# Performance work log

Measured on AMD Instinct MI355X. Metric: run time of the kernel, lower is better.

Reference implementation:

```python
import jax, jax.numpy as jnp
import numpy as np

B, H, W, C = 64, 32, 32, 256
HZ, WZ = 16, 16
N = 64          # hidden_dim = n_proposals
K = 3           # dynamic depthwise kernel size
EPS = 1e-5


def _layernorm(x, g, b):
    mu = jnp.mean(x, axis=-1, keepdims=True)
    var = jnp.var(x, axis=-1, keepdims=True)
    return (x - mu) * jax.lax.rsqrt(var + EPS) * g + b


def setup_inputs() -> dict:
    key = jax.random.key(0)
    ks = jax.random.split(key, 8)
    s = 0.02  # weight init scale
    return {
        "x_feat": jax.random.normal(ks[0], (B, H, W, C), jnp.float32),
        "z_feat": jax.random.normal(ks[1], (B, HZ, WZ, C), jnp.float32),
        "Wz": jax.random.normal(ks[2], (C, N), jnp.float32) * s,
        "bz": jnp.zeros((N,), jnp.float32),
        "Wx": jax.random.normal(ks[3], (C, N), jnp.float32) * s,
        "bx": jnp.zeros((N,), jnp.float32),
        "Wdyn": jax.random.normal(ks[4], (C, N + K), jnp.float32) * s,
        "bdyn": jnp.zeros((N + K,), jnp.float32),
        "g_norm": jnp.ones((C,), jnp.float32),
        "b_norm": jnp.zeros((C,), jnp.float32),
        "Wp": jax.random.normal(ks[5], (C, 1), jnp.float32) * s,
        "bp": jnp.zeros((1,), jnp.float32),
        "g_ln": jnp.ones((C,), jnp.float32),
        "b_ln": jnp.zeros((C,), jnp.float32),
    }


def _dysep_conv_atten(query, value, Wdyn, bdyn, g_norm, b_norm):
    # query, value: [B, N, C]
    dy = query @ Wdyn + bdyn                      # [B, N, N+K]
    w_depth = dy[:, :, :K]                        # [B, N, K] per-channel depthwise kernels
    w_point = dy[:, :, K:]                        # [B, N, N] per-sample pointwise (1x1) weights
    # depthwise conv along C with 'same' padding (torch conv1d = cross-correlation)
    vpad = jnp.pad(value, ((0, 0), (0, 0), (1, 1)))
    depth = (w_depth[..., 0:1] * vpad[:, :, 0:C]
             + w_depth[..., 1:2] * vpad[:, :, 1:C + 1]
             + w_depth[..., 2:3] * vpad[:, :, 2:C + 2])
    depth = jax.nn.relu(depth)                    # [B, N, C]
    point = jnp.einsum('bnm,bmc->bnc', w_point, depth)
    return _layernorm(point, g_norm, b_norm)


def reference(x_feat, z_feat, Wz, bz, Wx, bx, Wdyn, bdyn,
              g_norm, b_norm, Wp, bp, g_ln, b_ln):
    # kernels from template features (detached in the original: kernels.detach())
    z_core = z_feat @ Wz + bz                                   # [B,HZ,WZ,N]
    kernels = jnp.einsum('bhwn,bhwc->bnc', z_core, z_feat)      # [B,N,C]
    kernels = jax.lax.stop_gradient(kernels)

    x_n = x_feat @ Wx + bx                                      # [B,H,W,N]
    kernels_x = jnp.einsum('bhwn,bhwc->bnc', x_n, x_feat)       # [B,N,C]
    kernels_x = _dysep_conv_atten(kernels, kernels_x, Wdyn, bdyn, g_norm, b_norm)

    x_corr = jnp.einsum('bnc,bhwn->bhwc', kernels_x, x_n)       # [B,H,W,C]
    proto = kernels_x @ Wp + bp                                 # [B,N,1]
    tem = jax.nn.sigmoid(jnp.einsum('bnd,bnc->bdc', proto, kernels_x))  # [B,1,C]
    tem = tem[:, :, None, :]                                    # [B,1,1,C]
    x_corr = x_corr * tem

    return x_feat + jax.nn.relu(_layernorm(x_corr, g_ln, b_ln))
```

## Files before the change

### kernel.cpp

```cpp
#include <hip/hip_runtime.h>
#include <math.h>

#define EPSV 1e-5f

__global__ __launch_bounds__(256) void gemm_all(
    const float* __restrict__ Xx, const float* __restrict__ Wxp,
    const float* __restrict__ bxp, float* __restrict__ Yx,
    const float* __restrict__ Xz, const float* __restrict__ Wzp,
    const float* __restrict__ bzp, float* __restrict__ Yz)
{
    __shared__ float Xc[16][64];
    __shared__ float Wc[16][64];
    const int t = threadIdx.x;
    const float *X, *W, *bias; float* Y; long r0;
    if (blockIdx.x < 1024) { X = Xx; W = Wxp; bias = bxp; Y = Yx; r0 = (long)blockIdx.x * 64; }
    else                   { X = Xz; W = Wzp; bias = bzp; Y = Yz; r0 = (long)(blockIdx.x - 1024) * 64; }

    const int tr = t >> 4, tc = t & 15;
    float4 bv = *(const float4*)(bias + tc * 4);
    float acc[4][4];
#pragma unroll
    for (int i = 0; i < 4; ++i) { acc[i][0]=bv.x; acc[i][1]=bv.y; acc[i][2]=bv.z; acc[i][3]=bv.w; }

    const int lr = t >> 2, lc = (t & 3) * 4;
    const int wl = t >> 4, wj = (t & 15) * 4;
    float4 xv = *(const float4*)(X + (r0 + lr) * 256 + lc);
    float4 wv = *(const float4*)(W + (long)wl * 64 + wj);

    for (int c0 = 0; c0 < 256; c0 += 16) {
        Xc[lc + 0][lr] = xv.x; Xc[lc + 1][lr] = xv.y; Xc[lc + 2][lr] = xv.z; Xc[lc + 3][lr] = xv.w;
        *(float4*)&Wc[wl][wj] = wv;
        __syncthreads();
        if (c0 + 16 < 256) {
            xv = *(const float4*)(X + (r0 + lr) * 256 + c0 + 16 + lc);
            wv = *(const float4*)(W + (long)(c0 + 16 + wl) * 64 + wj);
        }
#pragma unroll
        for (int cl = 0; cl < 16; ++cl) {
            float4 a = *(float4*)&Xc[cl][tr * 4];
            float4 b = *(float4*)&Wc[cl][tc * 4];
            acc[0][0] += a.x * b.x; acc[0][1] += a.x * b.y; acc[0][2] += a.x * b.z; acc[0][3] += a.x * b.w;
            acc[1][0] += a.y * b.x; acc[1][1] += a.y * b.y; acc[1][2] += a.y * b.z; acc[1][3] += a.y * b.w;
            acc[2][0] += a.z * b.x; acc[2][1] += a.z * b.y; acc[2][2] += a.z * b.z; acc[2][3] += a.z * b.w;
            acc[3][0] += a.w * b.x; acc[3][1] += a.w * b.y; acc[3][2] += a.w * b.z; acc[3][3] += a.w * b.w;
        }
        __syncthreads();
    }
#pragma unroll
    for (int i = 0; i < 4; ++i) {
        float4 o = make_float4(acc[i][0], acc[i][1], acc[i][2], acc[i][3]);
        *(float4*)(Y + (r0 + tr * 4 + i) * 64 + tc * 4) = o;
    }
}

__global__ __launch_bounds__(256) void corr_all(
    const float* __restrict__ xn, const float* __restrict__ xf,
    float* __restrict__ kxr, const float* __restrict__ zc,
    const float* __restrict__ zf, float* __restrict__ kern)
{
    __shared__ float A[16 * 64];
    __shared__ float Bt[16 * 64];
    const int t = threadIdx.x;
    const float *Yn, *X; float* S; int b, P;
    if (blockIdx.y < 64) { b = blockIdx.y;      Yn = xn; X = xf; S = kxr;  P = 1024; }
    else                 { b = blockIdx.y - 64; Yn = zc; X = zf; S = kern; P = 256;  }
    const int c0 = blockIdx.x * 64;
    const int lp = t >> 4, lj = (t & 15) * 4;
    const int tn = t >> 4, tc = t & 15;

    float acc[4][4] = {};
    long rb = (long)b * P + lp;
    float4 av = *(const float4*)(Yn + rb * 64 + lj);
    float4 bv = *(const float4*)(X + rb * 256 + c0 + lj);

    for (int p0 = 0; p0 < P; p0 += 16) {
        *(float4*)&A[lp * 64 + lj] = av;
        *(float4*)&Bt[lp * 64 + lj] = bv;
        __syncthreads();
        if (p0 + 16 < P) {
            long rb2 = (long)b * P + p0 + 16 + lp;
            av = *(const float4*)(Yn + rb2 * 64 + lj);
            bv = *(const float4*)(X + rb2 * 256 + c0 + lj);
        }
#pragma unroll
        for (int p = 0; p < 16; ++p) {
            float4 a = *(float4*)&A[p * 64 + tn * 4];
            float4 b4 = *(float4*)&Bt[p * 64 + tc * 4];
            acc[0][0] += a.x * b4.x; acc[0][1] += a.x * b4.y; acc[0][2] += a.x * b4.z; acc[0][3] += a.x * b4.w;
            acc[1][0] += a.y * b4.x; acc[1][1] += a.y * b4.y; acc[1][2] += a.y * b4.z; acc[1][3] += a.y * b4.w;
            acc[2][0] += a.z * b4.x; acc[2][1] += a.z * b4.y; acc[2][2] += a.z * b4.z; acc[2][3] += a.z * b4.w;
            acc[3][0] += a.w * b4.x; acc[3][1] += a.w * b4.y; acc[3][2] += a.w * b4.z; acc[3][3] += a.w * b4.w;
        }
        __syncthreads();
    }
#pragma unroll
    for (int i = 0; i < 4; ++i) {
        float4 o = make_float4(acc[i][0], acc[i][1], acc[i][2], acc[i][3]);
        *(float4*)(S + ((long)(b * 64 + tn * 4 + i)) * 256 + c0 + tc * 4) = o;
    }
}

__global__ __launch_bounds__(256) void pointln_tem(
    const float* __restrict__ kern, const float* __restrict__ Wdyn,
    const float* __restrict__ bdyn, const float* __restrict__ v,
    const float* __restrict__ g, const float* __restrict__ bta,
    const float* __restrict__ Wp, const float* __restrict__ bp,
    float* __restrict__ pointbuf, float* __restrict__ kx,
    float* __restrict__ tem)
{
    __shared__ float wp[64][64];
    __shared__ float Ac[16][64];
    __shared__ float Wc[16][64];
    __shared__ float wd[64][4];
    __shared__ float red1[64][4], red2[64][4];
    __shared__ float mu[64], rr[64], proto[64];
    const int b = blockIdx.x, t = threadIdx.x;
    const int tr = t >> 4, tc = t & 15;

    {
        float acc[4][4];
#pragma unroll
        for (int j = 0; j < 4; ++j) {
            float bj = bdyn[3 + tc * 4 + j];
            acc[0][j] = bj; acc[1][j] = bj; acc[2][j] = bj; acc[3][j] = bj;
        }
        const int lr = t >> 2, lc = (t & 3) * 4;
        const int wl = t >> 4, wj = (t & 15) * 4;
        float4 av = *(const float4*)(kern + ((long)(b * 64 + lr)) * 256 + lc);
        float w0 = Wdyn[wl * 67 + 3 + wj + 0];
        float w1 = Wdyn[wl * 67 + 3 + wj + 1];
        float w2 = Wdyn[wl * 67 + 3 + wj + 2];
        float w3 = Wdyn[wl * 67 + 3 + wj + 3];
        for (int c0 = 0; c0 < 256; c0 += 16) {
            Ac[lc + 0][lr] = av.x; Ac[lc + 1][lr] = av.y; Ac[lc + 2][lr] = av.z; Ac[lc + 3][lr] = av.w;
            Wc[wl][wj + 0] = w0; Wc[wl][wj + 1] = w1; Wc[wl][wj + 2] = w2; Wc[wl][wj + 3] = w3;
            __syncthreads();
            if (c0 + 16 < 256) {
                av = *(const float4*)(kern + ((long)(b * 64 + lr)) * 256 + c0 + 16 + lc);
                w0 = Wdyn[(c0 + 16 + wl) * 67 + 3 + wj + 0];
                w1 = Wdyn[(c0 + 16 + wl) * 67 + 3 + wj + 1];
                w2 = Wdyn[(c0 + 16 + wl) * 67 + 3 + wj + 2];
                w3 = Wdyn[(c0 + 16 + wl) * 67 + 3 + wj + 3];
            }
#pragma unroll
            for (int cl = 0; cl < 16; ++cl) {
                float4 a = *(float4*)&Ac[cl][tr * 4];
                float4 w = *(float4*)&Wc[cl][tc * 4];
                acc[0][0] += a.x * w.x; acc[0][1] += a.x * w.y; acc[0][2] += a.x * w.z; acc[0][3] += a.x * w.w;
                acc[1][0] += a.y * w.x; acc[1][1] += a.y * w.y; acc[1][2] += a.y * w.z; acc[1][3] += a.y * w.w;
                acc[2][0] += a.z * w.x; acc[2][1] += a.z * w.y; acc[2][2] += a.z * w.z; acc[2][3] += a.z * w.w;
                acc[3][0] += a.w * w.x; acc[3][1] += a.w * w.y; acc[3][2] += a.w * w.z; acc[3][3] += a.w * w.w;
            }
            __syncthreads();
        }
#pragma unroll
        for (int i = 0; i < 4; ++i)
            *(float4*)&wp[tr * 4 + i][tc * 4] = make_float4(acc[i][0], acc[i][1], acc[i][2], acc[i][3]);
    }
    if (t < 192) {
        int n = t / 3, j = t - n * 3;
        const float* kr = kern + ((long)(b * 64 + n)) * 256;
        float a0 = 0.f, a1 = 0.f, a2 = 0.f, a3 = 0.f;
        for (int c = 0; c < 256; c += 4) {
            a0 += kr[c + 0] * Wdyn[(c + 0) * 67 + j];
            a1 += kr[c + 1] * Wdyn[(c + 1) * 67 + j];
            a2 += kr[c + 2] * Wdyn[(c + 2) * 67 + j];
            a3 += kr[c + 3] * Wdyn[(c + 3) * 67 + j];
        }
        wd[n][j] = a0 + a1 + a2 + a3 + bdyn[j];
    }
    __syncthreads();

    const int c = t;
    float dcol[64];
#pragma unroll
    for (int m = 0; m < 64; ++m) {
        const float* vr = v + ((long)(b * 64 + m)) * 256;
        float vm = (c > 0)   ? vr[c - 1] : 0.f;
        float v0 = vr[c];
        float vp = (c < 255) ? vr[c + 1] : 0.f;
        float d = wd[m][0] * vm + wd[m][1] * v0 + wd[m][2] * vp;
        dcol[m] = fmaxf(d, 0.f);
    }
#pragma unroll 4
    for (int n = 0; n < 64; ++n) {
        float a = 0.f;
#pragma unroll
        for (int m4 = 0; m4 < 16; ++m4) {
            float4 w = *(float4*)&wp[n][m4 * 4];
            a += w.x * dcol[m4 * 4 + 0] + w.y * dcol[m4 * 4 + 1]
               + w.z * dcol[m4 * 4 + 2] + w.w * dcol[m4 * 4 + 3];
        }
        pointbuf[((long)(b * 64 + n)) * 256 + c] = a;
    }
    __syncthreads();
    {
        int n = t >> 2, q = t & 3;
        const float* pr = pointbuf + ((long)(b * 64 + n)) * 256 + q * 64;
        float s = 0.f, s2 = 0.f;
        for (int k = 0; k < 64; ++k) { float x = pr[k]; s += x; s2 += x * x; }
        red1[n][q] = s; red2[n][q] = s2;
    }
    __syncthreads();
    if (t < 64) {
        float s  = red1[t][0] + red1[t][1] + red1[t][2] + red1[t][3];
        float s2 = red2[t][0] + red2[t][1] + red2[t][2] + red2[t][3];
        float m = s * (1.f / 256.f);
        mu[t] = m; rr[t] = rsqrtf(s2 * (1.f / 256.f) - m * m + EPSV);
    }
    __syncthreads();
    {
        float gc = g[c], bc = bta[c];
#pragma unroll 4
        for (int n = 0; n < 64; ++n) {
            long off = ((long)(b * 64 + n)) * 256 + c;
            kx[off] = (pointbuf[off] - mu[n]) * rr[n] * gc + bc;
        }
    }
    __syncthreads();
    {
        int n = t >> 2, q = t & 3;
        const float* kr = kx + ((long)(b * 64 + n)) * 256 + q * 64;
        const float* wr = Wp + q * 64;
        float s = 0.f;
        for (int k = 0; k < 64; ++k) s += kr[k] * wr[k];
        red1[n][q] = s;
    }
    __syncthreads();
    if (t < 64) proto[t] = red1[t][0] + red1[t][1] + red1[t][2] + red1[t][3] + bp[0];
    __syncthreads();
    {
        float s = 0.f;
#pragma unroll 4
        for (int n = 0; n < 64; ++n) s += proto[n] * kx[((long)(b * 64 + n)) * 256 + c];
        tem[b * 256 + c] = 1.f / (1.f + expf(-s));
    }
}

__global__ __launch_bounds__(256) void final_kernel(
    const float* __restrict__ xn, const float* __restrict__ kx,
    const float* __restrict__ tem, const float* __restrict__ xf,
    const float* __restrict__ g, const float* __restrict__ bt,
    float* __restrict__ out)
{
    __shared__ float xtT[64][68];
    __shared__ float kc[64][68];
    __shared__ float rs1[64][17], rs2[64][17];
    __shared__ float mu[64], rr[64];
    const int t = threadIdx.x;
    const int b = blockIdx.y;
    const int pg = blockIdx.x;
    const int tr = t >> 4;
    const int tc = t & 15;

    {
        int row = t >> 2, q = t & 3;
        const float* src = xn + ((long)(b * 1024 + pg * 64 + row)) * 64 + q * 16;
        float4 f0 = *(const float4*)(src + 0);
        float4 f1 = *(const float4*)(src + 4);
        float4 f2 = *(const float4*)(src + 8);
        float4 f3 = *(const float4*)(src + 12);
        int n0 = q * 16;
        xtT[n0 + 0][row] = f0.x; xtT[n0 + 1][row] = f0.y; xtT[n0 + 2][row] = f0.z; xtT[n0 + 3][row] = f0.w;
        xtT[n0 + 4][row] = f1.x; xtT[n0 + 5][row] = f1.y; xtT[n0 + 6][row] = f1.z; xtT[n0 + 7][row] = f1.w;
        xtT[n0 + 8][row] = f2.x; xtT[n0 + 9][row] = f2.y; xtT[n0 +10][row] = f2.z; xtT[n0 +11][row] = f2.w;
        xtT[n0 +12][row] = f3.x; xtT[n0 +13][row] = f3.y; xtT[n0 +14][row] = f3.z; xtT[n0 +15][row] = f3.w;
    }

    float4 xcv[4][4];
    float si[4] = {0.f, 0.f, 0.f, 0.f}, s2i[4] = {0.f, 0.f, 0.f, 0.f};
#pragma unroll
    for (int cc = 0; cc < 4; ++cc) {
        __syncthreads();
#pragma unroll
        for (int i = 0; i < 4; ++i) {
            int idx = t + i * 256;
            int n = idx >> 4, jq = idx & 15;
            *(float4*)&kc[n][jq * 4] =
                *(const float4*)(kx + ((long)(b * 64 + n)) * 256 + cc * 64 + jq * 4);
        }
        __syncthreads();
        float4 a0 = {0,0,0,0}, a1 = {0,0,0,0}, a2 = {0,0,0,0}, a3 = {0,0,0,0};
#pragma unroll 8
        for (int n = 0; n < 64; ++n) {
            float4 xv = *(float4*)&xtT[n][tr * 4];
            float4 kv = *(float4*)&kc[n][tc * 4];
            a0.x += xv.x * kv.x; a0.y += xv.x * kv.y; a0.z += xv.x * kv.z; a0.w += xv.x * kv.w;
            a1.x += xv.y * kv.x; a1.y += xv.y * kv.y; a1.z += xv.y * kv.z; a1.w += xv.y * kv.w;
            a2.x += xv.z * kv.x; a2.y += xv.z * kv.y; a2.z += xv.z * kv.z; a2.w += xv.z * kv.w;
            a3.x += xv.w * kv.x; a3.y += xv.w * kv.y; a3.z += xv.w * kv.z; a3.w += xv.w * kv.w;
        }
        float4 tv = *(const float4*)(tem + b * 256 + cc * 64 + tc * 4);
        a0.x *= tv.x; a0.y *= tv.y; a0.z *= tv.z; a0.w *= tv.w;
        a1.x *= tv.x; a1.y *= tv.y; a1.z *= tv.z; a1.w *= tv.w;
        a2.x *= tv.x; a2.y *= tv.y; a2.z *= tv.z; a2.w *= tv.w;
        a3.x *= tv.x; a3.y *= tv.y; a3.z *= tv.z; a3.w *= tv.w;
        xcv[cc][0] = a0; xcv[cc][1] = a1; xcv[cc][2] = a2; xcv[cc][3] = a3;
        si[0]  += a0.x + a0.y + a0.z + a0.w;  s2i[0] += a0.x*a0.x + a0.y*a0.y + a0.z*a0.z + a0.w*a0.w;
        si[1]  += a1.x + a1.y + a1.z + a1.w;  s2i[1] += a1.x*a1.x + a1.y*a1.y + a1.z*a1.z + a1.w*a1.w;
        si[2]  += a2.x + a2.y + a2.z + a2.w;  s2i[2] += a2.x*a2.x + a2.y*a2.y + a2.z*a2.z + a2.w*a2.w;
        si[3]  += a3.x + a3.y + a3.z + a3.w;  s2i[3] += a3.x*a3.x + a3.y*a3.y + a3.z*a3.z + a3.w*a3.w;
    }
#pragma unroll
    for (int i = 0; i < 4; ++i) { rs1[tr * 4 + i][tc] = si[i]; rs2[tr * 4 + i][tc] = s2i[i]; }
    __syncthreads();
    if (t < 64) {
        float s = 0.f, s2 = 0.f;
#pragma unroll
        for (int k = 0; k < 16; ++k) { s += rs1[t][k]; s2 += rs2[t][k]; }
        float m = s * (1.f / 256.f);
        mu[t] = m; rr[t] = rsqrtf(s2 * (1.f / 256.f) - m * m + EPSV);
    }
    __syncthreads();
#pragma unroll
    for (int cc = 0; cc < 4; ++cc) {
        int cb = cc * 64 + tc * 4;
        float4 g4 = *(const float4*)(g + cb);
        float4 b4 = *(const float4*)(bt + cb);
#pragma unroll
        for (int i = 0; i < 4; ++i) {
            int row = tr * 4 + i;
            float m = mu[row], r = rr[row];
            long grow = ((long)(b * 1024 + pg * 64 + row)) * 256;
            float4 xfv = *(const float4*)(xf + grow + cb);
            float4 a = xcv[cc][i];
            float4 o;
            o.x = xfv.x + fmaxf((a.x - m) * r * g4.x + b4.x, 0.f);
            o.y = xfv.y + fmaxf((a.y - m) * r * g4.y + b4.y, 0.f);
            o.z = xfv.z + fmaxf((a.z - m) * r * g4.z + b4.z, 0.f);
            o.w = xfv.w + fmaxf((a.w - m) * r * g4.w + b4.w, 0.f);
            *(float4*)(out + grow + cb) = o;
        }
    }
}

extern "C" void kernel_launch(void* const* d_in, const int* in_sizes, int n_in,
                              void* d_out, int out_size, void* d_ws, size_t ws_size,
                              hipStream_t stream)
{
    (void)in_sizes; (void)n_in; (void)out_size; (void)ws_size;
    const float* x_feat = (const float*)d_in[0];
    const float* z_feat = (const float*)d_in[1];
    const float* Wz     = (const float*)d_in[2];
    const float* bz     = (const float*)d_in[3];
    const float* Wx     = (const float*)d_in[4];
    const float* bx     = (const float*)d_in[5];
    const float* Wdyn   = (const float*)d_in[6];
    const float* bdyn   = (const float*)d_in[7];
    const float* g_norm = (const float*)d_in[8];
    const float* b_norm = (const float*)d_in[9];
    const float* Wp     = (const float*)d_in[10];
    const float* bp     = (const float*)d_in[11];
    const float* g_ln   = (const float*)d_in[12];
    const float* b_ln   = (const float*)d_in[13];
    float* out = (float*)d_out;

    float* ws   = (float*)d_ws;
    float* xn   = ws;
    float* zc   = xn + 4194304;
    float* kern = zc + 1048576;
    float* kxr  = kern + 1048576;
    float* kx   = kxr + 1048576;
    float* temb = kx + 1048576;

    gemm_all<<<1280, 256, 0, stream>>>(x_feat, Wx, bx, xn, z_feat, Wz, bz, zc);
    corr_all<<<dim3(4, 128), 256, 0, stream>>>(xn, x_feat, kxr, zc, z_feat, kern);
    pointln_tem<<<64, 256, 0, stream>>>(kern, Wdyn, bdyn, kxr, g_norm, b_norm,
                                        Wp, bp, zc, kx, temb);
    final_kernel<<<dim3(16, 64), 256, 0, stream>>>(xn, kx, temb, x_feat, g_ln, b_ln, out);
}
```

Baseline: 314.7 us.

## Split dynamic-conv stage into parallel kernels, fold layernorm and tem into final

The single 64-block pointln_tem kernel is replaced by three kernels: dy_all computes the dynamic weights, depthpoint runs the depthwise conv and pointwise GEMM over a 4x64 grid and emits partial row statistics, and lntem finishes the layernorm statistics and the sigmoid gate analytically as per-channel scale and shift. final_kernel now applies the layernorm and gate while it stages the kernels, so the normalized kx buffer is no longer materialized. gemm_all moves to 128-row tiles with 8x4 per-thread outputs, and corr_all stages 64-row K tiles instead of 16. The aim is more parallelism in the low-occupancy middle stage and fewer barriers and better reuse in the GEMMs, at the cost of two extra launches and larger shared-memory use.

New measurement: 324.6 us. 3.1% more time.

```diff
diff --git a/kernel.cpp b/kernel.cpp
--- a/kernel.cpp
+++ b/kernel.cpp
@@ -9,47 +9,58 @@
     const float* __restrict__ Xz, const float* __restrict__ Wzp,
     const float* __restrict__ bzp, float* __restrict__ Yz)
 {
-    __shared__ float Xc[16][64];
-    __shared__ float Wc[16][64];
+    __shared__ float Xc[16 * 132];
+    __shared__ float Wc[16 * 64];
     const int t = threadIdx.x;
     const float *X, *W, *bias; float* Y; long r0;
-    if (blockIdx.x < 1024) { X = Xx; W = Wxp; bias = bxp; Y = Yx; r0 = (long)blockIdx.x * 64; }
-    else                   { X = Xz; W = Wzp; bias = bzp; Y = Yz; r0 = (long)(blockIdx.x - 1024) * 64; }
+    if (blockIdx.x < 512) { X = Xx; W = Wxp; bias = bxp; Y = Yx; r0 = (long)blockIdx.x * 128; }
+    else                  { X = Xz; W = Wzp; bias = bzp; Y = Yz; r0 = (long)(blockIdx.x - 512) * 128; }
 
     const int tr = t >> 4, tc = t & 15;
     float4 bv = *(const float4*)(bias + tc * 4);
-    float acc[4][4];
-#pragma unroll
-    for (int i = 0; i < 4; ++i) { acc[i][0]=bv.x; acc[i][1]=bv.y; acc[i][2]=bv.z; acc[i][3]=bv.w; }
-
-    const int lr = t >> 2, lc = (t & 3) * 4;
+    float acc[8][4];
+#pragma unroll
+    for (int i = 0; i < 8; ++i) { acc[i][0]=bv.x; acc[i][1]=bv.y; acc[i][2]=bv.z; acc[i][3]=bv.w; }
+
+    const int lr = t >> 2;
+    const int lc = (t & 3) * 4;
     const int wl = t >> 4, wj = (t & 15) * 4;
-    float4 xv = *(const float4*)(X + (r0 + lr) * 256 + lc);
-    float4 wv = *(const float4*)(W + (long)wl * 64 + wj);
+    float4 xv0 = *(const float4*)(X + (r0 + lr) * 256 + lc);
+    float4 xv1 = *(const float4*)(X + (r0 + lr + 64) * 256 + lc);
+    float4 wv  = *(const float4*)(W + (long)wl * 64 + wj);
 
     for (int c0 = 0; c0 < 256; c0 += 16) {
-        Xc[lc + 0][lr] = xv.x; Xc[lc + 1][lr] = xv.y; Xc[lc + 2][lr] = xv.z; Xc[lc + 3][lr] = xv.w;
-        *(float4*)&Wc[wl][wj] = wv;
+        Xc[(lc+0)*132 + lr] = xv0.x; Xc[(lc+1)*132 + lr] = xv0.y;
+        Xc[(lc+2)*132 + lr] = xv0.z; Xc[(lc+3)*132 + lr] = xv0.w;
+        Xc[(lc+0)*132 + lr+64] = xv1.x; Xc[(lc+1)*132 + lr+64] = xv1.y;
+        Xc[(lc+2)*132 + lr+64] = xv1.z; Xc[(lc+3)*132 + lr+64] = xv1.w;
+        *(float4*)&Wc[wl * 64 + wj] = wv;
         __syncthreads();
         if (c0 + 16 < 256) {
-            xv = *(const float4*)(X + (r0 + lr) * 256 + c0 + 16 + lc);
-            wv = *(const float4*)(W + (long)(c0 + 16 + wl) * 64 + wj);
+            xv0 = *(const float4*)(X + (r0 + lr) * 256 + c0 + 16 + lc);
+            xv1 = *(const float4*)(X + (r0 + lr + 64) * 256 + c0 + 16 + lc);
+            wv  = *(const float4*)(W + (long)(c0 + 16 + wl) * 64 + wj);
         }
 #pragma unroll
         for (int cl = 0; cl < 16; ++cl) {
-            float4 a = *(float4*)&Xc[cl][tr * 4];
-            float4 b = *(float4*)&Wc[cl][tc * 4];
-            acc[0][0] += a.x * b.x; acc[0][1] += a.x * b.y; acc[0][2] += a.x * b.z; acc[0][3] += a.x * b.w;
-            acc[1][0] += a.y * b.x; acc[1][1] += a.y * b.y; acc[1][2] += a.y * b.z; acc[1][3] += a.y * b.w;
-            acc[2][0] += a.z * b.x; acc[2][1] += a.z * b.y; acc[2][2] += a.z * b.z; acc[2][3] += a.z * b.w;
-            acc[3][0] += a.w * b.x; acc[3][1] += a.w * b.y; acc[3][2] += a.w * b.z; acc[3][3] += a.w * b.w;
-        }
-        __syncthreads();
-    }
-#pragma unroll
-    for (int i = 0; i < 4; ++i) {
+            float4 a0 = *(float4*)&Xc[cl * 132 + tr * 8];
+            float4 a1 = *(float4*)&Xc[cl * 132 + tr * 8 + 4];
+            float4 b4 = *(float4*)&Wc[cl * 64 + tc * 4];
+            acc[0][0]+=a0.x*b4.x; acc[0][1]+=a0.x*b4.y; acc[0][2]+=a0.x*b4.z; acc[0][3]+=a0.x*b4.w;
+            acc[1][0]+=a0.y*b4.x; acc[1][1]+=a0.y*b4.y; acc[1][2]+=a0.y*b4.z; acc[1][3]+=a0.y*b4.w;
+            acc[2][0]+=a0.z*b4.x; acc[2][1]+=a0.z*b4.y; acc[2][2]+=a0.z*b4.z; acc[2][3]+=a0.z*b4.w;
+            acc[3][0]+=a0.w*b4.x; acc[3][1]+=a0.w*b4.y; acc[3][2]+=a0.w*b4.z; acc[3][3]+=a0.w*b4.w;
+            acc[4][0]+=a1.x*b4.x; acc[4][1]+=a1.x*b4.y; acc[4][2]+=a1.x*b4.z; acc[4][3]+=a1.x*b4.w;
+            acc[5][0]+=a1.y*b4.x; acc[5][1]+=a1.y*b4.y; acc[5][2]+=a1.y*b4.z; acc[5][3]+=a1.y*b4.w;
+            acc[6][0]+=a1.z*b4.x; acc[6][1]+=a1.z*b4.y; acc[6][2]+=a1.z*b4.z; acc[6][3]+=a1.z*b4.w;
+            acc[7][0]+=a1.w*b4.x; acc[7][1]+=a1.w*b4.y; acc[7][2]+=a1.w*b4.z; acc[7][3]+=a1.w*b4.w;
+        }
+        __syncthreads();
+    }
+#pragma unroll
+    for (int i = 0; i < 8; ++i) {
         float4 o = make_float4(acc[i][0], acc[i][1], acc[i][2], acc[i][3]);
-        *(float4*)(Y + (r0 + tr * 4 + i) * 64 + tc * 4) = o;
+        *(float4*)(Y + (r0 + tr * 8 + i) * 64 + tc * 4) = o;
     }
 }
 
@@ -58,38 +69,49 @@
     float* __restrict__ kxr, const float* __restrict__ zc,
     const float* __restrict__ zf, float* __restrict__ kern)
 {
-    __shared__ float A[16 * 64];
-    __shared__ float Bt[16 * 64];
+    __shared__ float A[64 * 64];
+    __shared__ float Bt[64 * 64];
     const int t = threadIdx.x;
     const float *Yn, *X; float* S; int b, P;
     if (blockIdx.y < 64) { b = blockIdx.y;      Yn = xn; X = xf; S = kxr;  P = 1024; }
     else                 { b = blockIdx.y - 64; Yn = zc; X = zf; S = kern; P = 256;  }
     const int c0 = blockIdx.x * 64;
-    const int lp = t >> 4, lj = (t & 15) * 4;
     const int tn = t >> 4, tc = t & 15;
 
     float acc[4][4] = {};
-    long rb = (long)b * P + lp;
-    float4 av = *(const float4*)(Yn + rb * 64 + lj);
-    float4 bv = *(const float4*)(X + rb * 256 + c0 + lj);
-
-    for (int p0 = 0; p0 < P; p0 += 16) {
-        *(float4*)&A[lp * 64 + lj] = av;
-        *(float4*)&Bt[lp * 64 + lj] = bv;
-        __syncthreads();
-        if (p0 + 16 < P) {
-            long rb2 = (long)b * P + p0 + 16 + lp;
-            av = *(const float4*)(Yn + rb2 * 64 + lj);
-            bv = *(const float4*)(X + rb2 * 256 + c0 + lj);
-        }
-#pragma unroll
-        for (int p = 0; p < 16; ++p) {
-            float4 a = *(float4*)&A[p * 64 + tn * 4];
+    float4 av[4], bv4[4];
+#pragma unroll
+    for (int i = 0; i < 4; ++i) {
+        int idx = t + i * 256; int p = idx >> 4, f4 = (idx & 15) * 4;
+        long rb = (long)b * P + p;
+        av[i]  = *(const float4*)(Yn + rb * 64 + f4);
+        bv4[i] = *(const float4*)(X + rb * 256 + c0 + f4);
+    }
+    for (int p0 = 0; p0 < P; p0 += 64) {
+#pragma unroll
+        for (int i = 0; i < 4; ++i) {
+            int idx = t + i * 256; int p = idx >> 4, f4 = (idx & 15) * 4;
+            *(float4*)&A[p * 64 + f4] = av[i];
+            *(float4*)&Bt[p * 64 + f4] = bv4[i];
+        }
+        __syncthreads();
+        if (p0 + 64 < P) {
+#pragma unroll
+            for (int i = 0; i < 4; ++i) {
+                int idx = t + i * 256; int p = idx >> 4, f4 = (idx & 15) * 4;
+                long rb = (long)b * P + p0 + 64 + p;
+                av[i]  = *(const float4*)(Yn + rb * 64 + f4);
+                bv4[i] = *(const float4*)(X + rb * 256 + c0 + f4);
+            }
+        }
+#pragma unroll 16
+        for (int p = 0; p < 64; ++p) {
+            float4 a  = *(float4*)&A[p * 64 + tn * 4];
             float4 b4 = *(float4*)&Bt[p * 64 + tc * 4];
-            acc[0][0] += a.x * b4.x; acc[0][1] += a.x * b4.y; acc[0][2] += a.x * b4.z; acc[0][3] += a.x * b4.w;
-            acc[1][0] += a.y * b4.x; acc[1][1] += a.y * b4.y; acc[1][2] += a.y * b4.z; acc[1][3] += a.y * b4.w;
-            acc[2][0] += a.z * b4.x; acc[2][1] += a.z * b4.y; acc[2][2] += a.z * b4.z; acc[2][3] += a.z * b4.w;
-            acc[3][0] += a.w * b4.x; acc[3][1] += a.w * b4.y; acc[3][2] += a.w * b4.z; acc[3][3] += a.w * b4.w;
+            acc[0][0]+=a.x*b4.x; acc[0][1]+=a.x*b4.y; acc[0][2]+=a.x*b4.z; acc[0][3]+=a.x*b4.w;
+            acc[1][0]+=a.y*b4.x; acc[1][1]+=a.y*b4.y; acc[1][2]+=a.y*b4.z; acc[1][3]+=a.y*b4.w;
+            acc[2][0]+=a.z*b4.x; acc[2][1]+=a.z*b4.y; acc[2][2]+=a.z*b4.z; acc[2][3]+=a.z*b4.w;
+            acc[3][0]+=a.w*b4.x; acc[3][1]+=a.w*b4.y; acc[3][2]+=a.w*b4.z; acc[3][3]+=a.w*b4.w;
         }
         __syncthreads();
     }
@@ -100,159 +122,247 @@
     }
 }
 
-__global__ __launch_bounds__(256) void pointln_tem(
+__global__ __launch_bounds__(256) void dy_all(
     const float* __restrict__ kern, const float* __restrict__ Wdyn,
-    const float* __restrict__ bdyn, const float* __restrict__ v,
+    const float* __restrict__ bdyn, float* __restrict__ dyb)
+{
+    __shared__ float Ac[16 * 64];
+    __shared__ float Wc[16 * 64];
+    __shared__ float Wd3[48];
+    const int b = blockIdx.x, t = threadIdx.x;
+    const int tr = t >> 4, tc = t & 15;
+    float acc[4][4];
+#pragma unroll
+    for (int j = 0; j < 4; ++j) {
+        float bj = bdyn[3 + tc * 4 + j];
+        acc[0][j] = bj; acc[1][j] = bj; acc[2][j] = bj; acc[3][j] = bj;
+    }
+    const int lr = t >> 2, lc = (t & 3) * 4;
+    const int wl = t >> 4, wj = (t & 15) * 4;
+    const int nwd = t / 3, jwd = t - nwd * 3;
+    float wdacc = 0.f;
+    float4 av = *(const float4*)(kern + ((long)(b * 64 + lr)) * 256 + lc);
+    float w0 = Wdyn[wl * 67 + 3 + wj + 0];
+    float w1 = Wdyn[wl * 67 + 3 + wj + 1];
+    float w2 = Wdyn[wl * 67 + 3 + wj + 2];
+    float w3 = Wdyn[wl * 67 + 3 + wj + 3];
+    float wdr = (t < 48) ? Wdyn[(t / 3) * 67 + (t % 3)] : 0.f;
+
+    for (int c0 = 0; c0 < 256; c0 += 16) {
+        Ac[(lc+0)*64 + lr] = av.x; Ac[(lc+1)*64 + lr] = av.y;
+        Ac[(lc+2)*64 + lr] = av.z; Ac[(lc+3)*64 + lr] = av.w;
+        Wc[wl*64 + wj+0] = w0; Wc[wl*64 + wj+1] = w1;
+        Wc[wl*64 + wj+2] = w2; Wc[wl*64 + wj+3] = w3;
+        if (t < 48) Wd3[t] = wdr;
+        __syncthreads();
+        if (c0 + 16 < 256) {
+            av = *(const float4*)(kern + ((long)(b * 64 + lr)) * 256 + c0 + 16 + lc);
+            w0 = Wdyn[(c0 + 16 + wl) * 67 + 3 + wj + 0];
+            w1 = Wdyn[(c0 + 16 + wl) * 67 + 3 + wj + 1];
+            w2 = Wdyn[(c0 + 16 + wl) * 67 + 3 + wj + 2];
+            w3 = Wdyn[(c0 + 16 + wl) * 67 + 3 + wj + 3];
+            if (t < 48) wdr = Wdyn[(c0 + 16 + t / 3) * 67 + (t % 3)];
+        }
+#pragma unroll
+        for (int cl = 0; cl < 16; ++cl) {
+            float4 a = *(float4*)&Ac[cl * 64 + tr * 4];
+            float4 w = *(float4*)&Wc[cl * 64 + tc * 4];
+            acc[0][0]+=a.x*w.x; acc[0][1]+=a.x*w.y; acc[0][2]+=a.x*w.z; acc[0][3]+=a.x*w.w;
+            acc[1][0]+=a.y*w.x; acc[1][1]+=a.y*w.y; acc[1][2]+=a.y*w.z; acc[1][3]+=a.y*w.w;
+            acc[2][0]+=a.z*w.x; acc[2][1]+=a.z*w.y; acc[2][2]+=a.z*w.z; acc[2][3]+=a.z*w.w;
+            acc[3][0]+=a.w*w.x; acc[3][1]+=a.w*w.y; acc[3][2]+=a.w*w.z; acc[3][3]+=a.w*w.w;
+        }
+        if (t < 192) {
+#pragma unroll
+            for (int cl = 0; cl < 16; ++cl)
+                wdacc += Ac[cl * 64 + nwd] * Wd3[cl * 3 + jwd];
+        }
+        __syncthreads();
+    }
+#pragma unroll
+    for (int i = 0; i < 4; ++i) {
+        float4 o = make_float4(acc[i][0], acc[i][1], acc[i][2], acc[i][3]);
+        *(float4*)(dyb + ((long)(b * 64 + tr * 4 + i)) * 68 + tc * 4) = o;
+    }
+    if (t < 192) dyb[((long)(b * 64 + nwd)) * 68 + 64 + jwd] = wdacc + bdyn[jwd];
+}
+
+__global__ __launch_bounds__(256) void depthpoint(
+    const float* __restrict__ dyb, const float* __restrict__ v,
+    const float* __restrict__ g, const float* __restrict__ Wp,
+    float* __restrict__ point, float* __restrict__ partials)
+{
+    __shared__ float smem[13312];
+    float* wpT = smem;
+    float* wd3 = smem + 4352;
+    float* vt  = smem + 4608;
+    float* dep = smem + 8960;
+    float* rs  = vt;
+
+    const int t = threadIdx.x;
+    const int b = blockIdx.y, ct = blockIdx.x, c0 = ct * 64;
+    const int tr = t >> 4, tc = t & 15;
+
+#pragma unroll
+    for (int i = 0; i < 4; ++i) {
+        int idx = t + i * 256; int n = idx >> 4, m0 = (idx & 15) * 4;
+        float4 w4 = *(const float4*)(dyb + ((long)(b * 64 + n)) * 68 + m0);
+        wpT[(m0+0)*68 + n] = w4.x; wpT[(m0+1)*68 + n] = w4.y;
+        wpT[(m0+2)*68 + n] = w4.z; wpT[(m0+3)*68 + n] = w4.w;
+    }
+    if (t < 64) {
+        long o = ((long)(b * 64 + t)) * 68 + 64;
+        wd3[t*4+0] = dyb[o+0]; wd3[t*4+1] = dyb[o+1]; wd3[t*4+2] = dyb[o+2];
+    }
+    {
+        int m = t >> 2, lc0 = (t & 3) * 17;
+#pragma unroll
+        for (int k = 0; k < 17; ++k) {
+            int lc = lc0 + k;
+            if (lc < 66) {
+                int c = c0 - 1 + lc;
+                vt[m * 68 + lc] = (c >= 0 && c < 256) ? v[((long)(b * 64 + m)) * 256 + c] : 0.f;
+            }
+        }
+    }
+    __syncthreads();
+#pragma unroll
+    for (int im = 0; im < 4; ++im) {
+        int m = tr * 4 + im;
+        float w0 = wd3[m*4+0], w1 = wd3[m*4+1], w2 = wd3[m*4+2];
+#pragma unroll
+        for (int jc = 0; jc < 4; ++jc) {
+            int cl = tc * 4 + jc;
+            float d = w0 * vt[m*68 + cl] + w1 * vt[m*68 + cl + 1] + w2 * vt[m*68 + cl + 2];
+            dep[m*68 + cl] = fmaxf(d, 0.f);
+        }
+    }
+    __syncthreads();
+    float acc[4][4] = {};
+#pragma unroll 16
+    for (int m = 0; m < 64; ++m) {
+        float4 a4 = *(float4*)&wpT[m * 68 + tr * 4];
+        float4 d4 = *(float4*)&dep[m * 68 + tc * 4];
+        acc[0][0]+=a4.x*d4.x; acc[0][1]+=a4.x*d4.y; acc[0][2]+=a4.x*d4.z; acc[0][3]+=a4.x*d4.w;
+        acc[1][0]+=a4.y*d4.x; acc[1][1]+=a4.y*d4.y; acc[1][2]+=a4.y*d4.z; acc[1][3]+=a4.y*d4.w;
+        acc[2][0]+=a4.z*d4.x; acc[2][1]+=a4.z*d4.y; acc[2][2]+=a4.z*d4.z; acc[2][3]+=a4.z*d4.w;
+        acc[3][0]+=a4.w*d4.x; acc[3][1]+=a4.w*d4.y; acc[3][2]+=a4.w*d4.z; acc[3][3]+=a4.w*d4.w;
+    }
+    int cg = c0 + tc * 4;
+    float4 g4  = *(const float4*)(g + cg);
+    float4 wp4 = *(const float4*)(Wp + cg);
+    float gw0 = g4.x*wp4.x, gw1 = g4.y*wp4.y, gw2 = g4.z*wp4.z, gw3 = g4.w*wp4.w;
+#pragma unroll
+    for (int i = 0; i < 4; ++i) {
+        float4 o = make_float4(acc[i][0], acc[i][1], acc[i][2], acc[i][3]);
+        *(float4*)(point + ((long)(b * 64 + tr * 4 + i)) * 256 + cg) = o;
+        float s  = o.x + o.y + o.z + o.w;
+        float s2 = o.x*o.x + o.y*o.y + o.z*o.z + o.w*o.w;
+        float dg = o.x*gw0 + o.y*gw1 + o.z*gw2 + o.w*gw3;
+        rs[0*1088 + (tr*4+i)*17 + tc] = s;
+        rs[1*1088 + (tr*4+i)*17 + tc] = s2;
+        rs[2*1088 + (tr*4+i)*17 + tc] = dg;
+    }
+    __syncthreads();
+    if (t < 64) {
+        float s = 0.f, s2 = 0.f, dg = 0.f;
+#pragma unroll
+        for (int j = 0; j < 16; ++j) {
+            s  += rs[t*17 + j];
+            s2 += rs[1088 + t*17 + j];
+            dg += rs[2176 + t*17 + j];
+        }
+        long base = ((long)(b * 4 + ct)) * 192;
+        partials[base + t]        = s;
+        partials[base + 64 + t]   = s2;
+        partials[base + 128 + t]  = dg;
+    }
+}
+
+__global__ __launch_bounds__(256) void lntem(
+    const float* __restrict__ partials, const float* __restrict__ point,
     const float* __restrict__ g, const float* __restrict__ bta,
     const float* __restrict__ Wp, const float* __restrict__ bp,
-    float* __restrict__ pointbuf, float* __restrict__ kx,
-    float* __restrict__ tem)
-{
-    __shared__ float wp[64][64];
-    __shared__ float Ac[16][64];
-    __shared__ float Wc[16][64];
-    __shared__ float wd[64][4];
-    __shared__ float red1[64][4], red2[64][4];
-    __shared__ float mu[64], rr[64], proto[64];
+    float* __restrict__ murr, float* __restrict__ AB)
+{
+    __shared__ float sA[256], sB[256];
+    __shared__ float wnv[64];
+    __shared__ float tot[4];
     const int b = blockIdx.x, t = threadIdx.x;
-    const int tr = t >> 4, tc = t & 15;
-
-    {
-        float acc[4][4];
-#pragma unroll
-        for (int j = 0; j < 4; ++j) {
-            float bj = bdyn[3 + tc * 4 + j];
-            acc[0][j] = bj; acc[1][j] = bj; acc[2][j] = bj; acc[3][j] = bj;
-        }
-        const int lr = t >> 2, lc = (t & 3) * 4;
-        const int wl = t >> 4, wj = (t & 15) * 4;
-        float4 av = *(const float4*)(kern + ((long)(b * 64 + lr)) * 256 + lc);
-        float w0 = Wdyn[wl * 67 + 3 + wj + 0];
-        float w1 = Wdyn[wl * 67 + 3 + wj + 1];
-        float w2 = Wdyn[wl * 67 + 3 + wj + 2];
-        float w3 = Wdyn[wl * 67 + 3 + wj + 3];
-        for (int c0 = 0; c0 < 256; c0 += 16) {
-            Ac[lc + 0][lr] = av.x; Ac[lc + 1][lr] = av.y; Ac[lc + 2][lr] = av.z; Ac[lc + 3][lr] = av.w;
-            Wc[wl][wj + 0] = w0; Wc[wl][wj + 1] = w1; Wc[wl][wj + 2] = w2; Wc[wl][wj + 3] = w3;
-            __syncthreads();
-            if (c0 + 16 < 256) {
-                av = *(const float4*)(kern + ((long)(b * 64 + lr)) * 256 + c0 + 16 + lc);
-                w0 = Wdyn[(c0 + 16 + wl) * 67 + 3 + wj + 0];
-                w1 = Wdyn[(c0 + 16 + wl) * 67 + 3 + wj + 1];
-                w2 = Wdyn[(c0 + 16 + wl) * 67 + 3 + wj + 2];
-                w3 = Wdyn[(c0 + 16 + wl) * 67 + 3 + wj + 3];
-            }
-#pragma unroll
-            for (int cl = 0; cl < 16; ++cl) {
-                float4 a = *(float4*)&Ac[cl][tr * 4];
-                float4 w = *(float4*)&Wc[cl][tc * 4];
-                acc[0][0] += a.x * w.x; acc[0][1] += a.x * w.y; acc[0][2] += a.x * w.z; acc[0][3] += a.x * w.w;
-                acc[1][0] += a.y * w.x; acc[1][1] += a.y * w.y; acc[1][2] += a.y * w.z; acc[1][3] += a.y * w.w;
-                acc[2][0] += a.z * w.x; acc[2][1] += a.z * w.y; acc[2][2] += a.z * w.z; acc[2][3] += a.z * w.w;
-                acc[3][0] += a.w * w.x; acc[3][1] += a.w * w.y; acc[3][2] += a.w * w.z; acc[3][3] += a.w * w.w;
-            }
-            __syncthreads();
-        }
-#pragma unroll
-        for (int i = 0; i < 4; ++i)
-            *(float4*)&wp[tr * 4 + i][tc * 4] = make_float4(acc[i][0], acc[i][1], acc[i][2], acc[i][3]);
-    }
-    if (t < 192) {
-        int n = t / 3, j = t - n * 3;
-        const float* kr = kern + ((long)(b * 64 + n)) * 256;
-        float a0 = 0.f, a1 = 0.f, a2 = 0.f, a3 = 0.f;
-        for (int c = 0; c < 256; c += 4) {
-            a0 += kr[c + 0] * Wdyn[(c + 0) * 67 + j];
-            a1 += kr[c + 1] * Wdyn[(c + 1) * 67 + j];
-            a2 += kr[c + 2] * Wdyn[(c + 2) * 67 + j];
-            a3 += kr[c + 3] * Wdyn[(c + 3) * 67 + j];
-        }
-        wd[n][j] = a0 + a1 + a2 + a3 + bdyn[j];
-    }
-    __syncthreads();
-
     const int c = t;
-    float dcol[64];
-#pragma unroll
-    for (int m = 0; m < 64; ++m) {
-        const float* vr = v + ((long)(b * 64 + m)) * 256;
-        float vm = (c > 0)   ? vr[c - 1] : 0.f;
-        float v0 = vr[c];
-        float vp = (c < 255) ? vr[c + 1] : 0.f;
-        float d = wd[m][0] * vm + wd[m][1] * v0 + wd[m][2] * vp;
-        dcol[m] = fmaxf(d, 0.f);
-    }
-#pragma unroll 4
-    for (int n = 0; n < 64; ++n) {
-        float a = 0.f;
-#pragma unroll
-        for (int m4 = 0; m4 < 16; ++m4) {
-            float4 w = *(float4*)&wp[n][m4 * 4];
-            a += w.x * dcol[m4 * 4 + 0] + w.y * dcol[m4 * 4 + 1]
-               + w.z * dcol[m4 * 4 + 2] + w.w * dcol[m4 * 4 + 3];
-        }
-        pointbuf[((long)(b * 64 + n)) * 256 + c] = a;
-    }
-    __syncthreads();
-    {
-        int n = t >> 2, q = t & 3;
-        const float* pr = pointbuf + ((long)(b * 64 + n)) * 256 + q * 64;
-        float s = 0.f, s2 = 0.f;
-        for (int k = 0; k < 64; ++k) { float x = pr[k]; s += x; s2 += x * x; }
-        red1[n][q] = s; red2[n][q] = s2;
-    }
-    __syncthreads();
+    float gc = g[c], bc = bta[c], wpc = Wp[c];
+    sA[t] = gc * wpc; sB[t] = bc * wpc;
+    __syncthreads();
+    for (int off = 128; off >= 1; off >>= 1) {
+        if (t < off) { sA[t] += sA[t+off]; sB[t] += sB[t+off]; }
+        __syncthreads();
+    }
+    if (t == 0) { tot[0] = sA[0]; tot[1] = sB[0] + bp[0]; }
+    __syncthreads();
+    float Sgw = tot[0], Sbw = tot[1];
+
+    float protoe = 0.f, mu = 0.f, rr = 0.f;
     if (t < 64) {
-        float s  = red1[t][0] + red1[t][1] + red1[t][2] + red1[t][3];
-        float s2 = red2[t][0] + red2[t][1] + red2[t][2] + red2[t][3];
-        float m = s * (1.f / 256.f);
-        mu[t] = m; rr[t] = rsqrtf(s2 * (1.f / 256.f) - m * m + EPSV);
-    }
-    __syncthreads();
-    {
-        float gc = g[c], bc = bta[c];
-#pragma unroll 4
-        for (int n = 0; n < 64; ++n) {
-            long off = ((long)(b * 64 + n)) * 256 + c;
-            kx[off] = (pointbuf[off] - mu[n]) * rr[n] * gc + bc;
-        }
-    }
-    __syncthreads();
-    {
-        int n = t >> 2, q = t & 3;
-        const float* kr = kx + ((long)(b * 64 + n)) * 256 + q * 64;
-        const float* wr = Wp + q * 64;
-        float s = 0.f;
-        for (int k = 0; k < 64; ++k) s += kr[k] * wr[k];
-        red1[n][q] = s;
-    }
-    __syncthreads();
-    if (t < 64) proto[t] = red1[t][0] + red1[t][1] + red1[t][2] + red1[t][3] + bp[0];
-    __syncthreads();
-    {
-        float s = 0.f;
-#pragma unroll 4
-        for (int n = 0; n < 64; ++n) s += proto[n] * kx[((long)(b * 64 + n)) * 256 + c];
-        tem[b * 256 + c] = 1.f / (1.f + expf(-s));
-    }
+        float S1 = 0.f, S2 = 0.f, Sdg = 0.f;
+#pragma unroll
+        for (int ct = 0; ct < 4; ++ct) {
+            long o = ((long)(b * 4 + ct)) * 192;
+            S1 += partials[o + t]; S2 += partials[o + 64 + t]; Sdg += partials[o + 128 + t];
+        }
+        mu = S1 * (1.f / 256.f);
+        float var = S2 * (1.f / 256.f) - mu * mu;
+        rr = rsqrtf(var + EPSV);
+        protoe = rr * (Sdg - mu * Sgw) + Sbw;
+        wnv[t] = protoe * rr;
+        murr[b * 128 + 2*t]     = rr;
+        murr[b * 128 + 2*t + 1] = -mu * rr;
+    }
+    __syncthreads();
+    sA[t] = (t < 64) ? protoe * rr * mu : 0.f;
+    sB[t] = (t < 64) ? protoe : 0.f;
+    __syncthreads();
+    for (int off = 128; off >= 1; off >>= 1) {
+        if (t < off) { sA[t] += sA[t+off]; sB[t] += sB[t+off]; }
+        __syncthreads();
+    }
+    if (t == 0) { tot[2] = sA[0]; tot[3] = sB[0]; }
+    __syncthreads();
+    float Bv = tot[2], Sv = tot[3];
+
+    const float* pcol = point + (long)b * 64 * 256 + c;
+    float a0 = 0.f, a1 = 0.f, a2 = 0.f, a3 = 0.f;
+#pragma unroll
+    for (int n = 0; n < 64; n += 4) {
+        a0 += wnv[n+0] * pcol[(n+0) * 256];
+        a1 += wnv[n+1] * pcol[(n+1) * 256];
+        a2 += wnv[n+2] * pcol[(n+2) * 256];
+        a3 += wnv[n+3] * pcol[(n+3) * 256];
+    }
+    float accA = a0 + a1 + a2 + a3;
+    float x = gc * (accA - Bv) + bc * Sv;
+    float temv = 1.f / (1.f + expf(-x));
+    AB[b * 512 + c]       = gc * temv;
+    AB[b * 512 + 256 + c] = bc * temv;
 }
 
 __global__ __launch_bounds__(256) void final_kernel(
-    const float* __restrict__ xn, const float* __restrict__ kx,
-    const float* __restrict__ tem, const float* __restrict__ xf,
-    const float* __restrict__ g, const float* __restrict__ bt,
-    float* __restrict__ out)
-{
-    __shared__ float xtT[64][68];
-    __shared__ float kc[64][68];
-    __shared__ float rs1[64][17], rs2[64][17];
+    const float* __restrict__ xn, const float* __restrict__ point,
+    const float* __restrict__ murr, const float* __restrict__ AB,
+    const float* __restrict__ xf, const float* __restrict__ g,
+    const float* __restrict__ bt, float* __restrict__ out)
+{
+    __shared__ float xtT[64 * 68];
+    __shared__ float kc[64 * 68];
+    __shared__ float rs1[64 * 17], rs2[64 * 17];
     __shared__ float mu[64], rr[64];
+    __shared__ float rq[128];
     const int t = threadIdx.x;
     const int b = blockIdx.y;
     const int pg = blockIdx.x;
     const int tr = t >> 4;
     const int tc = t & 15;
 
+    if (t < 128) rq[t] = murr[b * 128 + t];
     {
         int row = t >> 2, q = t & 3;
         const float* src = xn + ((long)(b * 1024 + pg * 64 + row)) * 64 + q * 16;
@@ -261,14 +371,14 @@
         float4 f2 = *(const float4*)(src + 8);
         float4 f3 = *(const float4*)(src + 12);
         int n0 = q * 16;
-        xtT[n0 + 0][row] = f0.x; xtT[n0 + 1][row] = f0.y; xtT[n0 + 2][row] = f0.z; xtT[n0 + 3][row] = f0.w;
-        xtT[n0 + 4][row] = f1.x; xtT[n0 + 5][row] = f1.y; xtT[n0 + 6][row] = f1.z; xtT[n0 + 7][row] = f1.w;
-        xtT[n0 + 8][row] = f2.x; xtT[n0 + 9][row] = f2.y; xtT[n0 +10][row] = f2.z; xtT[n0 +11][row] = f2.w;
-        xtT[n0 +12][row] = f3.x; xtT[n0 +13][row] = f3.y; xtT[n0 +14][row] = f3.z; xtT[n0 +15][row] = f3.w;
+        xtT[(n0+ 0)*68+row]=f0.x; xtT[(n0+ 1)*68+row]=f0.y; xtT[(n0+ 2)*68+row]=f0.z; xtT[(n0+ 3)*68+row]=f0.w;
+        xtT[(n0+ 4)*68+row]=f1.x; xtT[(n0+ 5)*68+row]=f1.y; xtT[(n0+ 6)*68+row]=f1.z; xtT[(n0+ 7)*68+row]=f1.w;
+        xtT[(n0+ 8)*68+row]=f2.x; xtT[(n0+ 9)*68+row]=f2.y; xtT[(n0+10)*68+row]=f2.z; xtT[(n0+11)*68+row]=f2.w;
+        xtT[(n0+12)*68+row]=f3.x; xtT[(n0+13)*68+row]=f3.y; xtT[(n0+14)*68+row]=f3.z; xtT[(n0+15)*68+row]=f3.w;
     }
 
     float4 xcv[4][4];
-    float si[4] = {0.f, 0.f, 0.f, 0.f}, s2i[4] = {0.f, 0.f, 0.f, 0.f};
+    float si[4] = {0.f,0.f,0.f,0.f}, s2i[4] = {0.f,0.f,0.f,0.f};
 #pragma unroll
     for (int cc = 0; cc < 4; ++cc) {
         __syncthreads();
@@ -276,38 +386,42 @@
         for (int i = 0; i < 4; ++i) {
             int idx = t + i * 256;
             int n = idx >> 4, jq = idx & 15;
-            *(float4*)&kc[n][jq * 4] =
-                *(const float4*)(kx + ((long)(b * 64 + n)) * 256 + cc * 64 + jq * 4);
+            int cb = cc * 64 + jq * 4;
+            float4 p4 = *(const float4*)(point + ((long)(b * 64 + n)) * 256 + cb);
+            float rn = rq[2*n], qn = rq[2*n + 1];
+            float4 A4 = *(const float4*)(AB + b * 512 + cb);
+            float4 B4 = *(const float4*)(AB + b * 512 + 256 + cb);
+            float4 kv;
+            kv.x = (p4.x * rn + qn) * A4.x + B4.x;
+            kv.y = (p4.y * rn + qn) * A4.y + B4.y;
+            kv.z = (p4.z * rn + qn) * A4.z + B4.z;
+            kv.w = (p4.w * rn + qn) * A4.w + B4.w;
+            *(float4*)&kc[n * 68 + jq * 4] = kv;
         }
         __syncthreads();
         float4 a0 = {0,0,0,0}, a1 = {0,0,0,0}, a2 = {0,0,0,0}, a3 = {0,0,0,0};
 #pragma unroll 8
         for (int n = 0; n < 64; ++n) {
-            float4 xv = *(float4*)&xtT[n][tr * 4];
-            float4 kv = *(float4*)&kc[n][tc * 4];
-            a0.x += xv.x * kv.x; a0.y += xv.x * kv.y; a0.z += xv.x * kv.z; a0.w += xv.x * kv.w;
-            a1.x += xv.y * kv.x; a1.y += xv.y * kv.y; a1.z += xv.y * kv.z; a1.w += xv.y * kv.w;
-            a2.x += xv.z * kv.x; a2.y += xv.z * kv.y; a2.z += xv.z * kv.z; a2.w += xv.z * kv.w;
-            a3.x += xv.w * kv.x; a3.y += xv.w * kv.y; a3.z += xv.w * kv.z; a3.w += xv.w * kv.w;
-        }
-        float4 tv = *(const float4*)(tem + b * 256 + cc * 64 + tc * 4);
-        a0.x *= tv.x; a0.y *= tv.y; a0.z *= tv.z; a0.w *= tv.w;
-        a1.x *= tv.x; a1.y *= tv.y; a1.z *= tv.z; a1.w *= tv.w;
-        a2.x *= tv.x; a2.y *= tv.y; a2.z *= tv.z; a2.w *= tv.w;
-        a3.x *= tv.x; a3.y *= tv.y; a3.z *= tv.z; a3.w *= tv.w;
+            float4 xv = *(float4*)&xtT[n * 68 + tr * 4];
+            float4 kv = *(float4*)&kc[n * 68 + tc * 4];
+            a0.x += xv.x*kv.x; a0.y += xv.x*kv.y; a0.z += xv.x*kv.z; a0.w += xv.x*kv.w;
+            a1.x += xv.y*kv.x; a1.y += xv.y*kv.y; a1.z += xv.y*kv.z; a1.w += xv.y*kv.w;
+            a2.x += xv.z*kv.x; a2.y += xv.z*kv.y; a2.z += xv.z*kv.z; a2.w += xv.z*kv.w;
+            a3.x += xv.w*kv.x; a3.y += xv.w*kv.y; a3.z += xv.w*kv.z; a3.w += xv.w*kv.w;
+        }
         xcv[cc][0] = a0; xcv[cc][1] = a1; xcv[cc][2] = a2; xcv[cc][3] = a3;
-        si[0]  += a0.x + a0.y + a0.z + a0.w;  s2i[0] += a0.x*a0.x + a0.y*a0.y + a0.z*a0.z + a0.w*a0.w;
-        si[1]  += a1.x + a1.y + a1.z + a1.w;  s2i[1] += a1.x*a1.x + a1.y*a1.y + a1.z*a1.z + a1.w*a1.w;
-        si[2]  += a2.x + a2.y + a2.z + a2.w;  s2i[2] += a2.x*a2.x + a2.y*a2.y + a2.z*a2.z + a2.w*a2.w;
-        si[3]  += a3.x + a3.y + a3.z + a3.w;  s2i[3] += a3.x*a3.x + a3.y*a3.y + a3.z*a3.z + a3.w*a3.w;
-    }
-#pragma unroll
-    for (int i = 0; i < 4; ++i) { rs1[tr * 4 + i][tc] = si[i]; rs2[tr * 4 + i][tc] = s2i[i]; }
+        si[0] += a0.x+a0.y+a0.z+a0.w;  s2i[0] += a0.x*a0.x+a0.y*a0.y+a0.z*a0.z+a0.w*a0.w;
+        si[1] += a1.x+a1.y+a1.z+a1.w;  s2i[1] += a1.x*a1.x+a1.y*a1.y+a1.z*a1.z+a1.w*a1.w;
+        si[2] += a2.x+a2.y+a2.z+a2.w;  s2i[2] += a2.x*a2.x+a2.y*a2.y+a2.z*a2.z+a2.w*a2.w;
+        si[3] += a3.x+a3.y+a3.z+a3.w;  s2i[3] += a3.x*a3.x+a3.y*a3.y+a3.z*a3.z+a3.w*a3.w;
+    }
+#pragma unroll
+    for (int i = 0; i < 4; ++i) { rs1[(tr*4+i)*17 + tc] = si[i]; rs2[(tr*4+i)*17 + tc] = s2i[i]; }
     __syncthreads();
     if (t < 64) {
         float s = 0.f, s2 = 0.f;
 #pragma unroll
-        for (int k = 0; k < 16; ++k) { s += rs1[t][k]; s2 += rs2[t][k]; }
+        for (int k = 0; k < 16; ++k) { s += rs1[t*17 + k]; s2 += rs2[t*17 + k]; }
         float m = s * (1.f / 256.f);
         mu[t] = m; rr[t] = rsqrtf(s2 * (1.f / 256.f) - m * m + EPSV);
     }
@@ -355,17 +469,21 @@
     const float* b_ln   = (const float*)d_in[13];
     float* out = (float*)d_out;
 
-    float* ws   = (float*)d_ws;
-    float* xn   = ws;
-    float* zc   = xn + 4194304;
-    float* kern = zc + 1048576;
-    float* kxr  = kern + 1048576;
-    float* kx   = kxr + 1048576;
-    float* temb = kx + 1048576;
-
-    gemm_all<<<1280, 256, 0, stream>>>(x_feat, Wx, bx, xn, z_feat, Wz, bz, zc);
+    float* ws       = (float*)d_ws;
+    float* xn       = ws;
+    float* zc       = xn + 4194304;
+    float* kern     = zc + 1048576;
+    float* kxr      = kern + 1048576;
+    float* point    = kxr + 1048576;
+    float* dyb      = point + 1048576;
+    float* partials = dyb + 278528;
+    float* murr     = partials + 49152;
+    float* AB       = murr + 8192;
+
+    gemm_all<<<640, 256, 0, stream>>>(x_feat, Wx, bx, xn, z_feat, Wz, bz, zc);
     corr_all<<<dim3(4, 128), 256, 0, stream>>>(xn, x_feat, kxr, zc, z_feat, kern);
-    pointln_tem<<<64, 256, 0, stream>>>(kern, Wdyn, bdyn, kxr, g_norm, b_norm,
-                                        Wp, bp, zc, kx, temb);
-    final_kernel<<<dim3(16, 64), 256, 0, stream>>>(xn, kx, temb, x_feat, g_ln, b_ln, out);
-}
+    dy_all<<<64, 256, 0, stream>>>(kern, Wdyn, bdyn, dyb);
+    depthpoint<<<dim3(4, 64), 256, 0, stream>>>(dyb, kxr, g_norm, Wp, point, partials);
+    lntem<<<64, 256, 0, stream>>>(partials, point, g_norm, b_norm, Wp, bp, murr, AB);
+    final_kernel<<<dim3(16, 64), 256, 0, stream>>>(xn, point, murr, AB, x_feat, g_ln, b_ln, out);
+}
```
